# Kernel tuning notes

Hardware: AMD Instinct MI355X
Metric: run time of the kernel (lower is better)

Reference implementation:

```python
import jax, jax.numpy as jnp
import numpy as np
import math

B, S, D, H, HD, FF, L, NS = 16, 512, 256, 8, 32, 1024, 2, 1024
THETA = 10000.0
EPS = 1e-5


def setup_inputs() -> dict:
    key = jax.random.key(0)
    ks = jax.random.split(key, 20)
    n = lambda i, shape: jax.random.normal(ks[i], shape, jnp.float32) * 0.02
    inp = {
        'values': jax.random.normal(ks[0], (B, S), jnp.float32),
        'dib': jax.random.uniform(ks[1], (B, S), jnp.float32),
        'gamma': jax.random.uniform(ks[2], (B, S), jnp.float32),
        'memory_type': jnp.ones((B, S), jnp.float32),
        'key_padding_mask': jnp.ones((B, S), dtype=bool),
        # input projection Linear(5, D)
        'in_w': n(3, (5, D)), 'in_b': jnp.zeros((D,), jnp.float32),
        # per-layer params stacked on leading L axis
        'ln1_s': jnp.ones((L, D), jnp.float32), 'ln1_b': jnp.zeros((L, D), jnp.float32),
        'qw': n(4, (L, D, D)), 'qb': jnp.zeros((L, D), jnp.float32),
        'kw': n(5, (L, D, D)), 'kb': jnp.zeros((L, D), jnp.float32),
        'vw': n(6, (L, D, D)), 'vb': jnp.zeros((L, D), jnp.float32),
        'ow': n(7, (L, D, D)), 'ob': jnp.zeros((L, D), jnp.float32),
        'ln2_s': jnp.ones((L, D), jnp.float32), 'ln2_b': jnp.zeros((L, D), jnp.float32),
        'ffw1': n(8, (L, D, FF)), 'ffb1': jnp.zeros((L, FF), jnp.float32),
        'ffw2': n(9, (L, FF, D)), 'ffb2': jnp.zeros((L, D), jnp.float32),
        'fn_s': jnp.ones((D,), jnp.float32), 'fn_b': jnp.zeros((D,), jnp.float32),
        # output head Linear(S*D, NS)
        'head_w': n(10, (S * D, NS)), 'head_b': jnp.zeros((NS,), jnp.float32),
    }
    return inp


def _layernorm(x, s, b):
    m = jnp.mean(x, axis=-1, keepdims=True)
    v = jnp.mean(jnp.square(x - m), axis=-1, keepdims=True)
    return (x - m) * jax.lax.rsqrt(v + EPS) * s + b


def _rotate_half(x):
    x1, x2 = jnp.split(x, 2, axis=-1)
    return jnp.concatenate((-x2, x1), axis=-1)


def _rope_tables():
    pos = jnp.arange(S, dtype=jnp.float32)
    inv_freq = 1.0 / (THETA ** (jnp.arange(0, HD, 2, dtype=jnp.float32) / HD))
    freqs = pos[:, None] * inv_freq[None, :]           # [S, HD/2]
    emb = jnp.concatenate((freqs, freqs), axis=-1)      # [S, HD]
    return jnp.cos(emb), jnp.sin(emb)


def _forward(values, dib, gamma, memory_type, key_padding_mask,
             in_w, in_b, ln1_s, ln1_b, qw, qb, kw, kb, vw, vb, ow, ob,
             ln2_s, ln2_b, ffw1, ffb1, ffw2, ffb2, fn_s, fn_b, head_w, head_b):
    # token features: (sign, magnitude, gamma, dib, memory_type in {-1,+1})
    sign = jnp.where(values >= 0, 1.0, -1.0)
    mt = memory_type * 2.0 - 1.0  # values in [0,1] -> signed encoding
    features = jnp.stack((sign, jnp.abs(values), gamma, dib, mt), axis=-1)  # [B,S,5]
    x = features @ in_w + in_b  # [B,S,D]

    cos, sin = _rope_tables()  # [S,HD]
    cos4 = cos[None, None]     # [1,1,S,HD]
    sin4 = sin[None, None]
    mask = key_padding_mask    # [B,S] bool
    neg = jnp.finfo(x.dtype).min
    scale = 1.0 / math.sqrt(HD)

    for l in range(L):
        h = _layernorm(x, ln1_s[l], ln1_b[l])
        q = (h @ qw[l] + qb[l]).reshape(B, S, H, HD).transpose(0, 2, 1, 3)  # [B,H,S,HD]
        k = (h @ kw[l] + kb[l]).reshape(B, S, H, HD).transpose(0, 2, 1, 3)
        v = (h @ vw[l] + vb[l]).reshape(B, S, H, HD).transpose(0, 2, 1, 3)
        q = q * cos4 + _rotate_half(q) * sin4
        k = k * cos4 + _rotate_half(k) * sin4
        scores = jnp.einsum('bhqd,bhkd->bhqk', q, k) * scale  # [B,H,S,S]
        scores = jnp.where(mask[:, None, None, :], scores, neg)
        attn = jax.nn.softmax(scores, axis=-1)
        ctx = jnp.einsum('bhqk,bhkd->bhqd', attn, v)
        ctx = ctx.transpose(0, 2, 1, 3).reshape(B, S, D)
        out = (ctx @ ow[l] + ob[l]) * mask[..., None].astype(x.dtype)
        x = x + out
        h2 = _layernorm(x, ln2_s[l], ln2_b[l])
        ff = jax.nn.gelu(h2 @ ffw1[l] + ffb1[l], approximate=False) @ ffw2[l] + ffb2[l]
        x = x + ff

    x = _layernorm(x, fn_s, fn_b)
    logits = x.reshape(B, S * D) @ head_w + head_b  # [B,NS]
    return logits


def reference(values, dib, gamma, memory_type, key_padding_mask,
              in_w, in_b, ln1_s, ln1_b, qw, qb, kw, kb, vw, vb, ow, ob,
              ln2_s, ln2_b, ffw1, ffb1, ffw2, ffb2, fn_s, fn_b, head_w, head_b):
    return _forward(values, dib, gamma, memory_type, key_padding_mask,
                    in_w, in_b, ln1_s, ln1_b, qw, qb, kw, kb, vw, vb, ow, ob,
                    ln2_s, ln2_b, ffw1, ffb1, ffw2, ffb2, fn_s, fn_b, head_w, head_b)
```

## Files before the change

kernel.cpp:

```cpp
#include <hip/hip_runtime.h>
#include <math.h>

#define BB 16
#define SS 512
#define DD 256
#define HH 8
#define HDIM 32
#define FFD 1024
#define NL 2
#define NSOUT 1024
#define SD (SS*DD)
#define ROWS (BB*SS)

#define HEAD_KC 256
#define HEAD_NCH 512

typedef __attribute__((ext_vector_type(8))) short short8;
typedef __attribute__((ext_vector_type(4))) float f32x4;

__device__ __forceinline__ unsigned short f2bf(float f) {
    union { float f; unsigned u; } c; c.f = f;
    unsigned u = c.u + 0x7fffu + ((c.u >> 16) & 1u);
    return (unsigned short)(u >> 16);
}

__global__ __launch_bounds__(256) void k_prep_all(
    const float* __restrict__ p_qw, const float* __restrict__ p_kw,
    const float* __restrict__ p_vw, const float* __restrict__ p_ow,
    const float* __restrict__ p_f1w, const float* __restrict__ p_f2w,
    unsigned short* __restrict__ wq, unsigned short* __restrict__ wk,
    unsigned short* __restrict__ wv, unsigned short* __restrict__ wo,
    unsigned short* __restrict__ wf1, unsigned short* __restrict__ wf2,
    float* __restrict__ ct, float* __restrict__ st,
    const float* __restrict__ values, const float* __restrict__ dib,
    const float* __restrict__ gamma, const float* __restrict__ mtyp,
    const float* __restrict__ in_w, const float* __restrict__ in_b,
    float* __restrict__ x) {
    int bid = blockIdx.x;
    int t = threadIdx.x;
    if (bid >= 1568) {
        int i = (bid - 1568) * 256 + t;
        int row = i >> 6, d4 = (i & 63) * 4;
        float v = values[row];
        float f0 = (v >= 0.f) ? 1.f : -1.f;
        float f1 = fabsf(v);
        float f2 = gamma[row];
        float f3 = dib[row];
        float f4 = mtyp[row] * 2.f - 1.f;
        float4 w0 = *(const float4*)&in_w[d4];
        float4 w1 = *(const float4*)&in_w[DD + d4];
        float4 w2 = *(const float4*)&in_w[2 * DD + d4];
        float4 w3 = *(const float4*)&in_w[3 * DD + d4];
        float4 w4 = *(const float4*)&in_w[4 * DD + d4];
        float4 bb = *(const float4*)&in_b[d4];
        float4 o;
        o.x = f0 * w0.x + f1 * w1.x + f2 * w2.x + f3 * w3.x + f4 * w4.x + bb.x;
        o.y = f0 * w0.y + f1 * w1.y + f2 * w2.y + f3 * w3.y + f4 * w4.y + bb.y;
        o.z = f0 * w0.z + f1 * w1.z + f2 * w2.z + f3 * w3.z + f4 * w4.z + bb.z;
        o.w = f0 * w0.w + f1 * w1.w + f2 * w2.w + f3 * w3.w + f4 * w4.w + bb.w;
        *(float4*)&x[(size_t)row * DD + d4] = o;
        return;
    }
    if (bid >= 1536) {
        int i = (bid - 1536) * 256 + t;
        if (i < SS * 16) {
            int s = i >> 4, f = i & 15;
            float invf = powf(10000.f, -(float)f / 16.f);
            float ang = (float)s * invf;
            ct[i] = cosf(ang);
            st[i] = sinf(ang);
        }
        return;
    }
    const float* src; unsigned short* dst;
    int K, N, kx, nx, l;
    if (bid < 512) {
        int grp = bid >> 7, r = bid & 127; l = r >> 6; int tl = r & 63;
        kx = tl >> 3; nx = tl & 7; K = DD; N = DD;
        src = grp == 0 ? p_qw : grp == 1 ? p_kw : grp == 2 ? p_vw : p_ow;
        dst = grp == 0 ? wq : grp == 1 ? wk : grp == 2 ? wv : wo;
    } else if (bid < 1024) {
        int r = bid - 512; l = r >> 8; int tl = r & 255;
        kx = tl >> 5; nx = tl & 31; K = DD; N = FFD; src = p_f1w; dst = wf1;
    } else {
        int r = bid - 1024; l = r >> 8; int tl = r & 255;
        kx = tl >> 3; nx = tl & 7; K = FFD; N = DD; src = p_f2w; dst = wf2;
    }
    __shared__ float tile[32][33];
    size_t zo = (size_t)l * K * N;
    int k0 = kx * 32, n0 = nx * 32;
    int r_ = t >> 3, c4 = (t & 7) * 4;
    float4 a = *(const float4*)&src[zo + (size_t)(k0 + r_) * N + n0 + c4];
    tile[r_][c4 + 0] = a.x; tile[r_][c4 + 1] = a.y; tile[r_][c4 + 2] = a.z; tile[r_][c4 + 3] = a.w;
    __syncthreads();
    unsigned o0 = f2bf(tile[c4 + 0][r_]), o1 = f2bf(tile[c4 + 1][r_]);
    unsigned o2 = f2bf(tile[c4 + 2][r_]), o3 = f2bf(tile[c4 + 3][r_]);
    uint2 ud = { o0 | (o1 << 16), o2 | (o3 << 16) };
    *(uint2*)&dst[zo + (size_t)(n0 + r_) * K + k0 + c4] = ud;
}

template <bool OBF>
__global__ __launch_bounds__(256) void k_layernorm_w(
    const float* __restrict__ in, void* __restrict__ outp,
    const float* __restrict__ sc, const float* __restrict__ bi) {
    int t = threadIdx.x, lane = t & 63, w = t >> 6;
    int row = blockIdx.x * 4 + w;
    float4 v = *(const float4*)&in[(size_t)row * DD + lane * 4];
    float s1 = v.x + v.y + v.z + v.w;
    float s2 = v.x * v.x + v.y * v.y + v.z * v.z + v.w * v.w;
#pragma unroll
    for (int off = 32; off > 0; off >>= 1) {
        s1 += __shfl_xor(s1, off);
        s2 += __shfl_xor(s2, off);
    }
    float mean = s1 * (1.f / DD);
    float var = s2 * (1.f / DD) - mean * mean;
    float rstd = rsqrtf(var + 1e-5f);
    float4 sv = *(const float4*)&sc[lane * 4];
    float4 bv = *(const float4*)&bi[lane * 4];
    float o0 = (v.x - mean) * rstd * sv.x + bv.x;
    float o1 = (v.y - mean) * rstd * sv.y + bv.y;
    float o2 = (v.z - mean) * rstd * sv.z + bv.z;
    float o3 = (v.w - mean) * rstd * sv.w + bv.w;
    if (OBF) {
        ushort4 u = { f2bf(o0), f2bf(o1), f2bf(o2), f2bf(o3) };
        *(ushort4*)&((unsigned short*)outp)[(size_t)row * DD + lane * 4] = u;
    } else {
        float4 o = { o0, o1, o2, o3 };
        *(float4*)&((float*)outp)[(size_t)row * DD + lane * 4] = o;
    }
}

__global__ __launch_bounds__(256) void k_gemm_ff1(
    const short* __restrict__ A, const short* __restrict__ Bt,
    const float* __restrict__ bias, unsigned short* __restrict__ Cout,
    int M, int N, int K) {
    __shared__ __align__(16) short As[128 * 32];
    __shared__ __align__(16) short Bs[128 * 32];
    int t = threadIdx.x;
    int lane = t & 63, wid = t >> 6;
    int wr = wid >> 1, wc = wid & 1;
    int m0 = blockIdx.x * 128, n0 = blockIdx.y * 128;
    f32x4 acc[4][4] = {};
    int srow = t >> 2, sslot = t & 3;
    for (int k0 = 0; k0 < K; k0 += 32) {
#pragma unroll
        for (int p = 0; p < 2; ++p) {
            int row = srow + p * 64;
            int sw = sslot ^ ((row >> 1) & 3);
            *(float4*)&As[row * 32 + sw * 8] =
                *(const float4*)&A[(size_t)(m0 + row) * K + k0 + sslot * 8];
            *(float4*)&Bs[row * 32 + sw * 8] =
                *(const float4*)&Bt[(size_t)(n0 + row) * K + k0 + sslot * 8];
        }
        __syncthreads();
        short8 af[4], bfr[4];
#pragma unroll
        for (int mt = 0; mt < 4; ++mt) {
            int row = wr * 64 + mt * 16 + (lane & 15);
            int sl = (lane >> 4) ^ ((row >> 1) & 3);
            af[mt] = *(const short8*)&As[row * 32 + sl * 8];
        }
#pragma unroll
        for (int nt = 0; nt < 4; ++nt) {
            int row = wc * 64 + nt * 16 + (lane & 15);
            int sl = (lane >> 4) ^ ((row >> 1) & 3);
            bfr[nt] = *(const short8*)&Bs[row * 32 + sl * 8];
        }
#pragma unroll
        for (int mt = 0; mt < 4; ++mt)
#pragma unroll
            for (int nt = 0; nt < 4; ++nt)
                acc[mt][nt] = __builtin_amdgcn_mfma_f32_16x16x32_bf16(af[mt], bfr[nt], acc[mt][nt], 0, 0, 0);
        __syncthreads();
    }
#pragma unroll
    for (int mt = 0; mt < 4; ++mt) {
#pragma unroll
        for (int i = 0; i < 4; ++i) {
            int gm = m0 + wr * 64 + mt * 16 + (lane >> 4) * 4 + i;
#pragma unroll
            for (int nt = 0; nt < 4; ++nt) {
                int gn = n0 + wc * 64 + nt * 16 + (lane & 15);
                float v = acc[mt][nt][i] + bias[gn];
                v = 0.5f * v * (1.f + erff(v * 0.70710678118654752f));
                Cout[(size_t)gm * N + gn] = f2bf(v);
            }
        }
    }
}

template <int EPI>
__global__ __launch_bounds__(256) void k_gemm64(
    const short* __restrict__ A, const short* __restrict__ Bt,
    const float* __restrict__ bias, float* __restrict__ Cout,
    int M, int N, int K, const float* __restrict__ resx, const int* __restrict__ mask) {
    __shared__ __align__(16) short As[64 * 64];
    __shared__ __align__(16) short Bs[128 * 64];
    int t = threadIdx.x;
    int lane = t & 63, wid = t >> 6;
    int wr = wid >> 1, wc = wid & 1;
    int m0 = blockIdx.x * 64, n0 = blockIdx.y * 128;
    int l15 = lane & 15, lh = lane >> 4;
    f32x4 acc[2][4] = {};
    for (int k0 = 0; k0 < K; k0 += 64) {
#pragma unroll
        for (int p = 0; p < 2; ++p) {
            int idx = t + p * 256;
            int row = idx >> 3, sl = idx & 7;
            int sw = sl ^ (row & 7);
            *(float4*)&As[row * 64 + sw * 8] =
                *(const float4*)&A[(size_t)(m0 + row) * K + k0 + sl * 8];
        }
#pragma unroll
        for (int p = 0; p < 4; ++p) {
            int idx = t + p * 256;
            int row = idx >> 3, sl = idx & 7;
            int sw = sl ^ (row & 7);
            *(float4*)&Bs[row * 64 + sw * 8] =
                *(const float4*)&Bt[(size_t)(n0 + row) * K + k0 + sl * 8];
        }
        __syncthreads();
#pragma unroll
        for (int kk = 0; kk < 2; ++kk) {
            short8 af[2], bfr[4];
#pragma unroll
            for (int mt = 0; mt < 2; ++mt) {
                int row = wr * 32 + mt * 16 + l15;
                int sl = (kk * 4 + lh) ^ (row & 7);
                af[mt] = *(const short8*)&As[row * 64 + sl * 8];
            }
#pragma unroll
            for (int nt = 0; nt < 4; ++nt) {
                int row = wc * 64 + nt * 16 + l15;
                int sl = (kk * 4 + lh) ^ (row & 7);
                bfr[nt] = *(const short8*)&Bs[row * 64 + sl * 8];
            }
#pragma unroll
            for (int mt = 0; mt < 2; ++mt)
#pragma unroll
                for (int nt = 0; nt < 4; ++nt)
                    acc[mt][nt] = __builtin_amdgcn_mfma_f32_16x16x32_bf16(af[mt], bfr[nt], acc[mt][nt], 0, 0, 0);
        }
        __syncthreads();
    }
#pragma unroll
    for (int mt = 0; mt < 2; ++mt) {
#pragma unroll
        for (int i = 0; i < 4; ++i) {
            int gm = m0 + wr * 32 + mt * 16 + lh * 4 + i;
            float mk = 1.f;
            if (EPI == 2) mk = (mask[gm] != 0) ? 1.f : 0.f;
#pragma unroll
            for (int nt = 0; nt < 4; ++nt) {
                int gn = n0 + wc * 64 + nt * 16 + l15;
                float v = acc[mt][nt][i] + bias[gn];
                v = resx[(size_t)gm * N + gn] + v * mk;
                Cout[(size_t)gm * N + gn] = v;
            }
        }
    }
}

__global__ __launch_bounds__(256) void k_qkv64(
    const short* __restrict__ A,
    const short* __restrict__ Wq, const short* __restrict__ Wk, const short* __restrict__ Wv,
    const float* __restrict__ bq, const float* __restrict__ bk, const float* __restrict__ bv,
    const float* __restrict__ ct, const float* __restrict__ st,
    unsigned short* __restrict__ q16, unsigned short* __restrict__ k16,
    unsigned short* __restrict__ vt16) {
    __shared__ __align__(16) short As[64 * 32];
    __shared__ __align__(16) short Bs[128 * 32];
    int mat = blockIdx.y >> 1;
    int n0 = (blockIdx.y & 1) * 128;
    const short* Bt = (mat == 0) ? Wq : (mat == 1) ? Wk : Wv;
    const float* bias = (mat == 0) ? bq : (mat == 1) ? bk : bv;
    int t = threadIdx.x;
    int lane = t & 63, wid = t >> 6;
    int wr = wid >> 1, wc = wid & 1;
    int m0 = blockIdx.x * 64;
    int l15 = lane & 15, lh = lane >> 4;
    f32x4 acc[2][4] = {};
    int srow = t >> 2, sslot = t & 3;
    for (int k0 = 0; k0 < DD; k0 += 32) {
        {
            int sw = sslot ^ ((srow >> 1) & 3);
            *(float4*)&As[srow * 32 + sw * 8] =
                *(const float4*)&A[(size_t)(m0 + srow) * DD + k0 + sslot * 8];
        }
#pragma unroll
        for (int p = 0; p < 2; ++p) {
            int row = srow + p * 64;
            int sw = sslot ^ ((row >> 1) & 3);
            *(float4*)&Bs[row * 32 + sw * 8] =
                *(const float4*)&Bt[(size_t)(n0 + row) * DD + k0 + sslot * 8];
        }
        __syncthreads();
        short8 af[2], bfr[4];
#pragma unroll
        for (int mt = 0; mt < 2; ++mt) {
            int row = wr * 32 + mt * 16 + l15;
            int sl = lh ^ ((row >> 1) & 3);
            af[mt] = *(const short8*)&As[row * 32 + sl * 8];
        }
#pragma unroll
        for (int nt = 0; nt < 4; ++nt) {
            int row = wc * 64 + nt * 16 + l15;
            int sl = lh ^ ((row >> 1) & 3);
            bfr[nt] = *(const short8*)&Bs[row * 32 + sl * 8];
        }
#pragma unroll
        for (int mt = 0; mt < 2; ++mt)
#pragma unroll
            for (int nt = 0; nt < 4; ++nt)
                acc[mt][nt] = __builtin_amdgcn_mfma_f32_16x16x32_bf16(af[mt], bfr[nt], acc[mt][nt], 0, 0, 0);
        __syncthreads();
    }
    float bs[4];
#pragma unroll
    for (int nt = 0; nt < 4; ++nt) bs[nt] = bias[n0 + wc * 64 + nt * 16 + l15];
    if (mat < 2) {
        unsigned short* dst = (mat == 0) ? q16 : k16;
        const float qscale = (mat == 0) ? 0.17677669529663687f : 1.f;
#pragma unroll
        for (int mt = 0; mt < 2; ++mt) {
#pragma unroll
            for (int i = 0; i < 4; ++i) {
                int gm = m0 + wr * 32 + mt * 16 + lh * 4 + i;
                int s = gm & (SS - 1);
                float c = ct[s * 16 + l15], sn = st[s * 16 + l15];
                float val[4];
#pragma unroll
                for (int nt = 0; nt < 4; ++nt) val[nt] = (acc[mt][nt][i] + bs[nt]) * qscale;
#pragma unroll
                for (int nt = 0; nt < 4; ++nt) {
                    float partner = val[nt ^ 1];
                    float o = ((nt & 1) == 0) ? (val[nt] * c - partner * sn)
                                              : (val[nt] * c + partner * sn);
                    dst[(size_t)gm * DD + n0 + wc * 64 + nt * 16 + l15] = f2bf(o);
                }
            }
        }
    } else {
#pragma unroll
        for (int mt = 0; mt < 2; ++mt) {
            int gmb = m0 + wr * 32 + mt * 16 + lh * 4;
            int b = gmb >> 9, sb = gmb & (SS - 1);
#pragma unroll
            for (int nt = 0; nt < 4; ++nt) {
                int gn = n0 + wc * 64 + nt * 16 + l15;
                int h = gn >> 5, d = gn & 31;
                ushort4 u;
#pragma unroll
                for (int i = 0; i < 4; ++i)
                    (&u.x)[i] = f2bf(acc[mt][nt][i] + bs[nt]);
                *(ushort4*)&vt16[((size_t)((b * HH + h) * HDIM + d)) * SS + sb] = u;
            }
        }
    }
}

__global__ __launch_bounds__(256) void k_flash(
    const short* __restrict__ qb, const short* __restrict__ kb,
    const short* __restrict__ vt, const int* __restrict__ mask,
    unsigned short* __restrict__ ctxb) {
    __shared__ float bias_lds[SS];
    __shared__ __align__(16) short p_lds[4][32 * 72];
    __shared__ __align__(16) float r_lds[4][32];
    int t = threadIdx.x, lane = t & 63, wq = t >> 6;
    int bh = blockIdx.y;
    int b = bh >> 3, h = bh & 7;
    int q0 = blockIdx.x * 128 + wq * 32;
    bias_lds[t]       = (mask[b * SS + t]       != 0) ? 0.f : -3.0e38f;
    bias_lds[t + 256] = (mask[b * SS + t + 256] != 0) ? 0.f : -3.0e38f;
    __syncthreads();
    int l15 = lane & 15, lh = lane >> 4;
    short8 qfr[2];
    qfr[0] = *(const short8*)&qb[((size_t)(b * SS) + q0 + l15) * DD + h * HDIM + lh * 8];
    qfr[1] = *(const short8*)&qb[((size_t)(b * SS) + q0 + 16 + l15) * DD + h * HDIM + lh * 8];
    float m[2] = {-3.0e38f, -3.0e38f};
    float lsum[2] = {0.f, 0.f};
    f32x4 oacc[2][2] = {};
    for (int k0 = 0; k0 < SS; k0 += 64) {
        f32x4 sT[4][2];
#pragma unroll
        for (int kt = 0; kt < 4; ++kt) {
            short8 kf = *(const short8*)&kb[((size_t)(b * SS) + k0 + kt * 16 + l15) * DD + h * HDIM + lh * 8];
#pragma unroll
            for (int qf = 0; qf < 2; ++qf) {
                f32x4 z = {0.f, 0.f, 0.f, 0.f};
                sT[kt][qf] = __builtin_amdgcn_mfma_f32_16x16x32_bf16(kf, qfr[qf], z, 0, 0, 0);
            }
        }
        float p[2][16];
        float r[2];
#pragma unroll
        for (int qf = 0; qf < 2; ++qf) {
            float pmax = -3.0e38f;
#pragma unroll
            for (int kt = 0; kt < 4; ++kt)
#pragma unroll
                for (int i = 0; i < 4; ++i) {
                    float s = sT[kt][qf][i] + bias_lds[k0 + kt * 16 + lh * 4 + i];
                    p[qf][kt * 4 + i] = s;
                    pmax = fmaxf(pmax, s);
                }
            pmax = fmaxf(pmax, __shfl_xor(pmax, 16));
            pmax = fmaxf(pmax, __shfl_xor(pmax, 32));
            float mn = fmaxf(m[qf], pmax);
            r[qf] = __expf(m[qf] - mn);
            m[qf] = mn;
            float cs = 0.f;
#pragma unroll
            for (int j = 0; j < 16; ++j) {
                float e = __expf(p[qf][j] - mn);
                p[qf][j] = e;
                cs += e;
            }
            cs += __shfl_xor(cs, 16);
            cs += __shfl_xor(cs, 32);
            lsum[qf] = lsum[qf] * r[qf] + cs;
        }
#pragma unroll
        for (int qf = 0; qf < 2; ++qf) {
            int qq = qf * 16 + l15;
#pragma unroll
            for (int kt = 0; kt < 4; ++kt) {
                unsigned u0 = (unsigned)f2bf(p[qf][kt * 4 + 0]) | ((unsigned)f2bf(p[qf][kt * 4 + 1]) << 16);
                unsigned u1 = (unsigned)f2bf(p[qf][kt * 4 + 2]) | ((unsigned)f2bf(p[qf][kt * 4 + 3]) << 16);
                uint2 u = { u0, u1 };
                *(uint2*)&p_lds[wq][qq * 72 + kt * 16 + lh * 4] = u;
            }
        }
        if (lane < 16) { r_lds[wq][l15] = r[0]; r_lds[wq][16 + l15] = r[1]; }
        __syncthreads();
#pragma unroll
        for (int mf = 0; mf < 2; ++mf) {
            float4 rv = *(const float4*)&r_lds[wq][mf * 16 + lh * 4];
#pragma unroll
            for (int df = 0; df < 2; ++df) {
                oacc[mf][df][0] *= rv.x; oacc[mf][df][1] *= rv.y;
                oacc[mf][df][2] *= rv.z; oacc[mf][df][3] *= rv.w;
            }
        }
#pragma unroll
        for (int ks = 0; ks < 2; ++ks) {
            short8 pa0 = *(const short8*)&p_lds[wq][(l15) * 72 + ks * 32 + lh * 8];
            short8 pa1 = *(const short8*)&p_lds[wq][(16 + l15) * 72 + ks * 32 + lh * 8];
#pragma unroll
            for (int df = 0; df < 2; ++df) {
                short8 vf = *(const short8*)&vt[((size_t)bh * HDIM + df * 16 + l15) * SS + k0 + ks * 32 + lh * 8];
                oacc[0][df] = __builtin_amdgcn_mfma_f32_16x16x32_bf16(pa0, vf, oacc[0][df], 0, 0, 0);
                oacc[1][df] = __builtin_amdgcn_mfma_f32_16x16x32_bf16(pa1, vf, oacc[1][df], 0, 0, 0);
            }
        }
        __syncthreads();
    }
    if (lane < 16) { r_lds[wq][l15] = 1.f / lsum[0]; r_lds[wq][16 + l15] = 1.f / lsum[1]; }
    __syncthreads();
#pragma unroll
    for (int mf = 0; mf < 2; ++mf) {
        float4 lv = *(const float4*)&r_lds[wq][mf * 16 + lh * 4];
        const float li[4] = { lv.x, lv.y, lv.z, lv.w };
#pragma unroll
        for (int df = 0; df < 2; ++df)
#pragma unroll
            for (int i = 0; i < 4; ++i) {
                int gq = q0 + mf * 16 + lh * 4 + i;
                int gd = df * 16 + l15;
                ctxb[((size_t)(b * SS) + gq) * DD + h * HDIM + gd] = f2bf(oacc[mf][df][i] * li[i]);
            }
    }
}

__global__ __launch_bounds__(256) void k_head_part(
    const float* __restrict__ x, const float* __restrict__ fns, const float* __restrict__ fnb,
    const float* __restrict__ W, float* __restrict__ part) {
    __shared__ float xs[16 * HEAD_KC];
    int c = blockIdx.x;
    int t = threadIdx.x, lane = t & 63, w = t >> 6;
    float4 sv = *(const float4*)&fns[lane * 4];
    float4 bv = *(const float4*)&fnb[lane * 4];
#pragma unroll
    for (int rr = 0; rr < 4; ++rr) {
        int b = w * 4 + rr;
        float4 v = *(const float4*)&x[(size_t)b * SD + c * HEAD_KC + lane * 4];
        float s1 = v.x + v.y + v.z + v.w;
        float s2 = v.x * v.x + v.y * v.y + v.z * v.z + v.w * v.w;
#pragma unroll
        for (int off = 32; off > 0; off >>= 1) {
            s1 += __shfl_xor(s1, off);
            s2 += __shfl_xor(s2, off);
        }
        float mean = s1 * (1.f / DD);
        float var = s2 * (1.f / DD) - mean * mean;
        float rstd = rsqrtf(var + 1e-5f);
        float4 o;
        o.x = (v.x - mean) * rstd * sv.x + bv.x;
        o.y = (v.y - mean) * rstd * sv.y + bv.y;
        o.z = (v.z - mean) * rstd * sv.z + bv.z;
        o.w = (v.w - mean) * rstd * sv.w + bv.w;
        *(float4*)&xs[b * HEAD_KC + lane * 4] = o;
    }
    __syncthreads();
    int k0 = c * HEAD_KC;
    int n4 = t * 4;
    float acc[16][4] = {};
#pragma unroll 8
    for (int k = 0; k < HEAD_KC; ++k) {
        f32x4 wv = __builtin_nontemporal_load((const f32x4*)&W[(size_t)(k0 + k) * NSOUT + n4]);
#pragma unroll
        for (int b = 0; b < 16; ++b) {
            float xv = xs[b * HEAD_KC + k];
            acc[b][0] += xv * wv[0]; acc[b][1] += xv * wv[1];
            acc[b][2] += xv * wv[2]; acc[b][3] += xv * wv[3];
        }
    }
#pragma unroll
    for (int b = 0; b < 16; ++b) {
        float4 o = {acc[b][0], acc[b][1], acc[b][2], acc[b][3]};
        *(float4*)&part[((size_t)c * 16 + b) * NSOUT + n4] = o;
    }
}

__global__ __launch_bounds__(512) void k_head_reduce(
    const float* __restrict__ part, const float* __restrict__ hb,
    float* __restrict__ out) {
    __shared__ float red[8][260];
    int t = threadIdx.x;
    int col = t & 63;
    int grp = t >> 6;
    int base = blockIdx.x * 256;
    f32x4 s = {0.f, 0.f, 0.f, 0.f};
#pragma unroll 8
    for (int c = grp; c < HEAD_NCH; c += 8) {
        f32x4 p = *(const f32x4*)&part[(size_t)c * (16 * NSOUT) + base + col * 4];
        s[0] += p[0]; s[1] += p[1]; s[2] += p[2]; s[3] += p[3];
    }
    red[grp][col * 4 + 0] = s[0];
    red[grp][col * 4 + 1] = s[1];
    red[grp][col * 4 + 2] = s[2];
    red[grp][col * 4 + 3] = s[3];
    __syncthreads();
    if (t < 256) {
        float acc = 0.f;
#pragma unroll
        for (int g = 0; g < 8; ++g) acc += red[g][t];
        out[base + t] = acc + hb[(base + t) & (NSOUT - 1)];
    }
}

extern "C" void kernel_launch(void* const* d_in, const int* in_sizes, int n_in,
                              void* d_out, int out_size, void* d_ws, size_t ws_size,
                              hipStream_t stream) {
    const float* values = (const float*)d_in[0];
    const float* dib    = (const float*)d_in[1];
    const float* gamma  = (const float*)d_in[2];
    const float* mtyp   = (const float*)d_in[3];
    const int*   mask   = (const int*)d_in[4];
    const float* in_w   = (const float*)d_in[5];
    const float* in_b   = (const float*)d_in[6];
    const float* ln1_s  = (const float*)d_in[7];
    const float* ln1_b  = (const float*)d_in[8];
    const float* p_qw   = (const float*)d_in[9];
    const float* p_qb   = (const float*)d_in[10];
    const float* p_kw   = (const float*)d_in[11];
    const float* p_kb   = (const float*)d_in[12];
    const float* p_vw   = (const float*)d_in[13];
    const float* p_vb   = (const float*)d_in[14];
    const float* p_ow   = (const float*)d_in[15];
    const float* p_ob   = (const float*)d_in[16];
    const float* ln2_s  = (const float*)d_in[17];
    const float* ln2_b  = (const float*)d_in[18];
    const float* p_f1w  = (const float*)d_in[19];
    const float* p_f1b  = (const float*)d_in[20];
    const float* p_f2w  = (const float*)d_in[21];
    const float* p_f2b  = (const float*)d_in[22];
    const float* fn_s   = (const float*)d_in[23];
    const float* fn_b   = (const float*)d_in[24];
    const float* head_w = (const float*)d_in[25];
    const float* head_b = (const float*)d_in[26];
    float* out = (float*)d_out;

    const size_t MB = 1u << 20;
    char* w = (char*)d_ws;
    float* x    = (float*)(w + 0 * MB);
    unsigned short* h16  = (unsigned short*)(w + 32 * MB);
    unsigned short* q16  = (unsigned short*)(w + 36 * MB);
    unsigned short* k16  = (unsigned short*)(w + 40 * MB);
    unsigned short* vt16 = (unsigned short*)(w + 44 * MB);
    unsigned short* cx16 = (unsigned short*)(w + 48 * MB);
    unsigned short* f116 = (unsigned short*)(w + 52 * MB);
    unsigned short* wq16 = (unsigned short*)(w + 68 * MB);
    unsigned short* wk16 = (unsigned short*)(w + 68 * MB + 256 * 1024);
    unsigned short* wv16 = (unsigned short*)(w + 68 * MB + 512 * 1024);
    unsigned short* wo16 = (unsigned short*)(w + 68 * MB + 768 * 1024);
    unsigned short* wf116 = (unsigned short*)(w + 69 * MB);
    unsigned short* wf216 = (unsigned short*)(w + 70 * MB);
    float* ct   = (float*)(w + 71 * MB);
    float* st   = (float*)(w + 71 * MB + 64 * 1024);
    float* sc   = (float*)(w + 72 * MB);

    k_prep_all<<<3616, 256, 0, stream>>>(p_qw, p_kw, p_vw, p_ow, p_f1w, p_f2w,
                                         wq16, wk16, wv16, wo16, wf116, wf216, ct, st,
                                         values, dib, gamma, mtyp, in_w, in_b, x);

    for (int l = 0; l < NL; ++l) {
        k_layernorm_w<true><<<2048, 256, 0, stream>>>(x, h16, ln1_s + l * DD, ln1_b + l * DD);
        k_qkv64<<<dim3(128, 6), 256, 0, stream>>>((const short*)h16,
            (const short*)(wq16 + l * 65536), (const short*)(wk16 + l * 65536),
            (const short*)(wv16 + l * 65536),
            p_qb + l * DD, p_kb + l * DD, p_vb + l * DD, ct, st, q16, k16, vt16);
        k_flash<<<dim3(4, BB * HH), 256, 0, stream>>>((const short*)q16, (const short*)k16,
            (const short*)vt16, mask, cx16);
        k_gemm64<2><<<dim3(128, 2), 256, 0, stream>>>((const short*)cx16,
            (const short*)(wo16 + l * 65536), p_ob + l * DD, x, ROWS, DD, DD, x, mask);
        k_layernorm_w<true><<<2048, 256, 0, stream>>>(x, h16, ln2_s + l * DD, ln2_b + l * DD);
        k_gemm_ff1<<<dim3(64, 8), 256, 0, stream>>>((const short*)h16,
            (const short*)(wf116 + l * 262144), p_f1b + l * FFD, f116, ROWS, FFD, DD);
        k_gemm64<3><<<dim3(128, 2), 256, 0, stream>>>((const short*)f116,
            (const short*)(wf216 + l * 262144), p_f2b + l * DD, x, ROWS, DD, FFD, x, nullptr);
    }

    k_head_part<<<HEAD_NCH, 256, 0, stream>>>(x, fn_s, fn_b, head_w, sc);
    k_head_reduce<<<64, 512, 0, stream>>>(sc, head_b, out);
}
```

Before: 342.3 us.

## Prefetch GEMM tiles into registers, use exp2 softmax and packed bf16 conversion

The 64x128 GEMM now loads the next K-tile from global memory into registers while the current tile is being multiplied, so load latency overlaps the MFMA work. The attention path folds log2(e) into the Q scale so softmax can use exp2f directly, and it replaces the software float-to-bf16 rounding with the hardware packed conversion instruction. The sentinel values are reduced so they stay finite under the base-2 scaling. The prefetch adds register pressure, which may lower occupancy.

```diff
diff --git a/kernel.cpp b/kernel.cpp
--- a/kernel.cpp
+++ b/kernel.cpp
@@ -203,24 +203,50 @@
     int m0 = blockIdx.x * 64, n0 = blockIdx.y * 128;
     int l15 = lane & 15, lh = lane >> 4;
     f32x4 acc[2][4] = {};
+    float4 ra[2], rb[4];
+#pragma unroll
+    for (int p = 0; p < 2; ++p) {
+        int idx = t + p * 256;
+        int row = idx >> 3, sl = idx & 7;
+        ra[p] = *(const float4*)&A[(size_t)(m0 + row) * K + sl * 8];
+    }
+#pragma unroll
+    for (int p = 0; p < 4; ++p) {
+        int idx = t + p * 256;
+        int row = idx >> 3, sl = idx & 7;
+        rb[p] = *(const float4*)&Bt[(size_t)(n0 + row) * K + sl * 8];
+    }
     for (int k0 = 0; k0 < K; k0 += 64) {
 #pragma unroll
         for (int p = 0; p < 2; ++p) {
             int idx = t + p * 256;
             int row = idx >> 3, sl = idx & 7;
             int sw = sl ^ (row & 7);
-            *(float4*)&As[row * 64 + sw * 8] =
-                *(const float4*)&A[(size_t)(m0 + row) * K + k0 + sl * 8];
+            *(float4*)&As[row * 64 + sw * 8] = ra[p];
         }
 #pragma unroll
         for (int p = 0; p < 4; ++p) {
             int idx = t + p * 256;
             int row = idx >> 3, sl = idx & 7;
             int sw = sl ^ (row & 7);
-            *(float4*)&Bs[row * 64 + sw * 8] =
-                *(const float4*)&Bt[(size_t)(n0 + row) * K + k0 + sl * 8];
-        }
-        __syncthreads();
+            *(float4*)&Bs[row * 64 + sw * 8] = rb[p];
+        }
+        __syncthreads();
+        int kn = k0 + 64;
+        if (kn < K) {
+#pragma unroll
+            for (int p = 0; p < 2; ++p) {
+                int idx = t + p * 256;
+                int row = idx >> 3, sl = idx & 7;
+                ra[p] = *(const float4*)&A[(size_t)(m0 + row) * K + kn + sl * 8];
+            }
+#pragma unroll
+            for (int p = 0; p < 4; ++p) {
+                int idx = t + p * 256;
+                int row = idx >> 3, sl = idx & 7;
+                rb[p] = *(const float4*)&Bt[(size_t)(n0 + row) * K + kn + sl * 8];
+            }
+        }
 #pragma unroll
         for (int kk = 0; kk < 2; ++kk) {
             short8 af[2], bfr[4];
@@ -321,7 +347,7 @@
     for (int nt = 0; nt < 4; ++nt) bs[nt] = bias[n0 + wc * 64 + nt * 16 + l15];
     if (mat < 2) {
         unsigned short* dst = (mat == 0) ? q16 : k16;
-        const float qscale = (mat == 0) ? 0.17677669529663687f : 1.f;
+        const float qscale = (mat == 0) ? 0.25503486f : 1.f;
 #pragma unroll
         for (int mt = 0; mt < 2; ++mt) {
 #pragma unroll
@@ -371,14 +397,14 @@
     int bh = blockIdx.y;
     int b = bh >> 3, h = bh & 7;
     int q0 = blockIdx.x * 128 + wq * 32;
-    bias_lds[t]       = (mask[b * SS + t]       != 0) ? 0.f : -3.0e38f;
-    bias_lds[t + 256] = (mask[b * SS + t + 256] != 0) ? 0.f : -3.0e38f;
+    bias_lds[t]       = (mask[b * SS + t]       != 0) ? 0.f : -1.0e38f;
+    bias_lds[t + 256] = (mask[b * SS + t + 256] != 0) ? 0.f : -1.0e38f;
     __syncthreads();
     int l15 = lane & 15, lh = lane >> 4;
     short8 qfr[2];
     qfr[0] = *(const short8*)&qb[((size_t)(b * SS) + q0 + l15) * DD + h * HDIM + lh * 8];
     qfr[1] = *(const short8*)&qb[((size_t)(b * SS) + q0 + 16 + l15) * DD + h * HDIM + lh * 8];
-    float m[2] = {-3.0e38f, -3.0e38f};
+    float m[2] = {-1.0e38f, -1.0e38f};
     float lsum[2] = {0.f, 0.f};
     f32x4 oacc[2][2] = {};
     for (int k0 = 0; k0 < SS; k0 += 64) {
@@ -396,7 +422,7 @@
         float r[2];
 #pragma unroll
         for (int qf = 0; qf < 2; ++qf) {
-            float pmax = -3.0e38f;
+            float pmax = -1.0e38f;
 #pragma unroll
             for (int kt = 0; kt < 4; ++kt)
 #pragma unroll
@@ -408,12 +434,12 @@
             pmax = fmaxf(pmax, __shfl_xor(pmax, 16));
             pmax = fmaxf(pmax, __shfl_xor(pmax, 32));
             float mn = fmaxf(m[qf], pmax);
-            r[qf] = __expf(m[qf] - mn);
+            r[qf] = exp2f(m[qf] - mn);
             m[qf] = mn;
             float cs = 0.f;
 #pragma unroll
             for (int j = 0; j < 16; ++j) {
-                float e = __expf(p[qf][j] - mn);
+                float e = exp2f(p[qf][j] - mn);
                 p[qf][j] = e;
                 cs += e;
             }
@@ -426,8 +452,11 @@
             int qq = qf * 16 + l15;
 #pragma unroll
             for (int kt = 0; kt < 4; ++kt) {
-                unsigned u0 = (unsigned)f2bf(p[qf][kt * 4 + 0]) | ((unsigned)f2bf(p[qf][kt * 4 + 1]) << 16);
-                unsigned u1 = (unsigned)f2bf(p[qf][kt * 4 + 2]) | ((unsigned)f2bf(p[qf][kt * 4 + 3]) << 16);
+                unsigned u0, u1;
+                asm("v_cvt_pk_bf16_f32 %0, %1, %2"
+                    : "=v"(u0) : "v"(p[qf][kt * 4 + 0]), "v"(p[qf][kt * 4 + 1]));
+                asm("v_cvt_pk_bf16_f32 %0, %1, %2"
+                    : "=v"(u1) : "v"(p[qf][kt * 4 + 2]), "v"(p[qf][kt * 4 + 3]));
                 uint2 u = { u0, u1 };
                 *(uint2*)&p_lds[wq][qq * 72 + kt * 16 + lh * 4] = u;
             }
```

Result: slower. 388.1 us (+13.4%).
